# Optimization experiments

Hardware: AMD Instinct MI355X
Metric: run time of the kernel (lower is better)

## Reference

```python
import jax, jax.numpy as jnp
import numpy as np

B = 512
MIRROR_C1_OFFSET = -1.2432432432432432

def make_ff(batch):
    ff = jnp.zeros((1, 1, 60, 60), jnp.float32)
    ff = ff.at[0, 0, :, 41:51].set(0.5)
    ff = ff.at[0, 0, :, 51:].set(1.0)
    return jnp.broadcast_to(ff, (batch, 1, 60, 60))

def conv_valid(x, w, b):
    y = jax.lax.conv_general_dilated(x, w, (1, 1), 'VALID',
                                     dimension_numbers=('NCHW', 'OIHW', 'NCHW'))
    return y + b[None, :, None, None]

def build_padded(x, h, ff):
    # (B,3,92,92) canvas with custom mirror padding (channel-dependent sign on left)
    b = x.shape[0]
    inner = jnp.concatenate([x, h, ff], axis=1)  # (B,3,60,60)
    h2 = jnp.zeros((b, 3, 92, 92), x.dtype)
    h2 = h2.at[:, :, 16:76, 16:76].set(inner)
    h2 = h2.at[:, :, 16:76, 76:].set(h2[:, :, 16:76, 60:76][..., ::-1])
    h2 = h2.at[:, :, 76:, 16:].set(h2[:, :, 60:76, 16:][:, :, ::-1, :])
    h2 = h2.at[:, :, :16, 16:].set(0.0)
    left = h2[:, :, :, 16:32][..., ::-1]  # mirror across col 16
    h2 = h2.at[:, 0, :, :16].set(left[:, 0])
    h2 = h2.at[:, 2, :, :16].set(left[:, 2])
    h2 = h2.at[:, 1, :, :16].set(MIRROR_C1_OFFSET - left[:, 1])
    return h2

def powerlayer(x, h, ff, w1, b1, w2, b2, w3, b3, w4, b4):
    h2 = build_padded(x, h, ff)
    h2 = jax.nn.relu(conv_valid(h2, w1, b1))  # (B,8,84,84)
    h2 = jax.nn.relu(conv_valid(h2, w2, b2))  # (B,8,76,76)
    h2 = jax.nn.relu(conv_valid(h2, w3, b3))  # (B,8,68,68)
    h2 = conv_valid(h2, w4, b4)               # (B,1,60,60)
    return h2

def setup_inputs() -> dict:
    key = jax.random.key(0)
    ks = jax.random.split(key, 10)
    x = jax.random.normal(ks[0], (B, 1, 60, 60), jnp.float32)
    fc_w = jax.random.normal(ks[1], (3600, 3600), jnp.float32) * (1.0 / 60.0)
    fc_b = jax.random.normal(ks[2], (3600,), jnp.float32) * 0.01
    w1 = jax.random.normal(ks[3], (8, 3, 9, 9), jnp.float32) * (1.0 / np.sqrt(3 * 81))
    bC1 = jnp.zeros((8,), jnp.float32)
    w2 = jax.random.normal(ks[4], (8, 8, 9, 9), jnp.float32) * (1.0 / np.sqrt(8 * 81))
    bC2 = jnp.zeros((8,), jnp.float32)
    w3 = jax.random.normal(ks[5], (8, 8, 9, 9), jnp.float32) * (1.0 / np.sqrt(8 * 81))
    bC3 = jnp.zeros((8,), jnp.float32)
    w4 = jax.random.normal(ks[6], (1, 8, 9, 9), jnp.float32) * (1.0 / np.sqrt(8 * 81))
    bC4 = jnp.zeros((1,), jnp.float32)
    return {"x": x, "fc_w": fc_w, "fc_b": fc_b,
            "w1": w1, "bC1": bC1, "w2": w2, "bC2": bC2,
            "w3": w3, "bC3": bC3, "w4": w4, "bC4": bC4}

def reference(x, fc_w, fc_b, w1, bC1, w2, bC2, w3, bC3, w4, bC4):
    b = x.shape[0]
    ff = make_ff(b)
    h = jax.nn.relu(x.reshape(b, 3600) @ fc_w.T + fc_b)
    h = h.reshape(b, 1, 60, 60)
    for _ in range(5):
        h = powerlayer(x, h, ff, w1, bC1, w2, bC2, w3, bC3, w4, bC4)
    return h.reshape(b, 60, 60)
```

## Files before the change

kernel.cpp:

```cpp
#include <hip/hip_runtime.h>

#define B_IMG 512
#define C1OFF (-1.2432432432432432f)

typedef __attribute__((ext_vector_type(2))) float f2;
typedef __attribute__((ext_vector_type(4))) float f4;
typedef __attribute__((ext_vector_type(4), aligned(4))) float f4u;

__device__ __forceinline__ float relu_(float v) { return v > 0.f ? v : 0.f; }
__device__ __forceinline__ f2 mk2(float a, float b) { f2 r; r[0] = a; r[1] = b; return r; }

__device__ __forceinline__ int swz_block(int bid, int nwg) {
    int q = nwg >> 3, r = nwg & 7;
    int xcd = bid & 7, idx = bid >> 3;
    return (xcd < r ? xcd * (q + 1) : r * (q + 1) + (xcd - r) * q) + idx;
}

__device__ __forceinline__ f2 pk_fma_sb0(f2 acc, f2 a, f2 b) {
    asm("v_pk_fma_f32 %0, %1, %2, %0 op_sel:[0,0,0] op_sel_hi:[0,1,1]"
        : "+v"(acc) : "s"(a), "v"(b));
    return acc;
}
__device__ __forceinline__ f2 pk_fma_sb1(f2 acc, f2 a, f2 b) {
    asm("v_pk_fma_f32 %0, %1, %2, %0 op_sel:[1,0,0] op_sel_hi:[1,1,1]"
        : "+v"(acc) : "s"(a), "v"(b));
    return acc;
}
__device__ __forceinline__ f2 pk_fma_vb0(f2 acc, f2 a, f2 b) {
    asm("v_pk_fma_f32 %0, %1, %2, %0 op_sel:[0,0,0] op_sel_hi:[0,1,1]"
        : "+v"(acc) : "v"(a), "v"(b));
    return acc;
}
__device__ __forceinline__ f2 pk_fma_vb1(f2 acc, f2 a, f2 b) {
    asm("v_pk_fma_f32 %0, %1, %2, %0 op_sel:[1,0,0] op_sel_hi:[1,1,1]"
        : "+v"(acc) : "v"(a), "v"(b));
    return acc;
}

#define KSPLIT 5
#define KCH 720

__global__ __launch_bounds__(256) void fc_split(
    const float* __restrict__ X, const float* __restrict__ W,
    float* __restrict__ P)
{
    __shared__ __align__(16) float As[16][68];
    __shared__ __align__(16) float Bs[16][68];
    const int tid = threadIdx.x;
    const int m0 = blockIdx.y * 64;
    const int n0 = blockIdx.x * 64;
    const int ks = blockIdx.z;
    const int kbeg = ks * KCH;
    const int tm = tid >> 4, tn = tid & 15;
    const int lr = tid >> 2;
    const int lk = (tid & 3) << 2;
    const bool bvalid = (n0 + lr) < 3600;
    const float* Arow = X + (size_t)(m0 + lr) * 3600 + lk;
    const float* Brow = W + (size_t)(bvalid ? (n0 + lr) : 0) * 3600 + lk;
    f2 acc2[4][2] = {};
    for (int k0 = kbeg; k0 < kbeg + KCH; k0 += 16) {
        float4 av = *(const float4*)(Arow + k0);
        float4 bv = make_float4(0.f, 0.f, 0.f, 0.f);
        if (bvalid) bv = *(const float4*)(Brow + k0);
        __syncthreads();
        As[lk + 0][lr] = av.x; As[lk + 1][lr] = av.y;
        As[lk + 2][lr] = av.z; As[lk + 3][lr] = av.w;
        Bs[lk + 0][lr] = bv.x; Bs[lk + 1][lr] = bv.y;
        Bs[lk + 2][lr] = bv.z; Bs[lk + 3][lr] = bv.w;
        __syncthreads();
        #pragma unroll
        for (int kk = 0; kk < 16; ++kk) {
            f2 a01 = *(const f2*)&As[kk][tm << 2];
            f2 a23 = *(const f2*)&As[kk][(tm << 2) + 2];
            f2 b01 = *(const f2*)&Bs[kk][tn << 2];
            f2 b23 = *(const f2*)&Bs[kk][(tn << 2) + 2];
            acc2[0][0] = pk_fma_vb0(acc2[0][0], a01, b01);
            acc2[0][1] = pk_fma_vb0(acc2[0][1], a01, b23);
            acc2[1][0] = pk_fma_vb1(acc2[1][0], a01, b01);
            acc2[1][1] = pk_fma_vb1(acc2[1][1], a01, b23);
            acc2[2][0] = pk_fma_vb0(acc2[2][0], a23, b01);
            acc2[2][1] = pk_fma_vb0(acc2[2][1], a23, b23);
            acc2[3][0] = pk_fma_vb1(acc2[3][0], a23, b01);
            acc2[3][1] = pk_fma_vb1(acc2[3][1], a23, b23);
        }
    }
    float* Pk = P + (size_t)ks * 512 * 3600;
    #pragma unroll
    for (int i = 0; i < 4; ++i) {
        int m = m0 + (tm << 2) + i;
        float vals[4] = { acc2[i][0][0], acc2[i][0][1],
                          acc2[i][1][0], acc2[i][1][1] };
        #pragma unroll
        for (int j = 0; j < 4; ++j) {
            int n = n0 + (tn << 2) + j;
            if (n < 3600)
                Pk[(size_t)m * 3600 + n] = vals[j];
        }
    }
}

__global__ __launch_bounds__(256) void fc_reduce(
    const float* __restrict__ P, const float* __restrict__ Bv,
    float* __restrict__ H)
{
    const size_t TOT = (size_t)512 * 3600;
    size_t i4 = (size_t)blockIdx.x * 256 + threadIdx.x;
    if (i4 >= TOT / 4) return;
    size_t off = i4 * 4;
    f4 s = *(const f4*)(P + off);
    #pragma unroll
    for (int ks = 1; ks < KSPLIT; ++ks) {
        f4 v = *(const f4*)(P + (size_t)ks * TOT + off);
        s[0] += v[0]; s[1] += v[1]; s[2] += v[2]; s[3] += v[3];
    }
    int n = (int)(off % 3600);
    f4u bv = *(const f4u*)(Bv + n);
    s[0] = relu_(s[0] + bv[0]); s[1] = relu_(s[1] + bv[1]);
    s[2] = relu_(s[2] + bv[2]); s[3] = relu_(s[3] + bv[3]);
    *(f4*)(H + off) = s;
}

__global__ __launch_bounds__(256) void prep_pk(
    const float* __restrict__ w, int OC, int IC, f2* __restrict__ out)
{
    int n = IC * 9 * OC * 5;
    for (int t = threadIdx.x + blockIdx.x * 256; t < n; t += gridDim.x * 256) {
        int m = t % 5; int rest = t / 5;
        int oc = rest % OC; rest /= OC;
        int ky = rest % 9; int ic = rest / 9;
        const float* ws = w + (((size_t)oc * IC + ic) * 9 + ky) * 9;
        float lo = ws[2 * m];
        float hi = (2 * m + 1 < 9) ? ws[2 * m + 1] : 0.f;
        out[t] = mk2(lo, hi);
    }
}

__device__ __forceinline__ float pad_core(const float* __restrict__ xb,
                                          const float* __restrict__ hb,
                                          int ch, int r, int c)
{
    if (r < 16) return 0.f;
    int rr = (r <= 75) ? r : (151 - r);
    int cc = (c <= 75) ? c : (151 - c);
    int i = rr - 16, j = cc - 16;
    if (ch == 0) return xb[i * 60 + j];
    if (ch == 1) return hb[i * 60 + j];
    return (j >= 51) ? 1.0f : ((j >= 41) ? 0.5f : 0.0f);
}

__device__ __forceinline__ float pad_val(const float* __restrict__ xb,
                                         const float* __restrict__ hb,
                                         int ch, int r, int c)
{
    if (c >= 16) return pad_core(xb, hb, ch, r, c);
    float v = pad_core(xb, hb, ch, r, 31 - c);
    return (ch == 1) ? (C1OFF - v) : v;
}

#define PADN 25392
#define CH1OFF 8464

__global__ __launch_bounds__(256) void pad02_kernel(
    const float* __restrict__ x, float* __restrict__ pad)
{
    const int b = blockIdx.x;
    const float* xb = x + (size_t)b * 3600;
    float* pb = pad + (size_t)b * PADN;
    for (int i = threadIdx.x; i < 2 * 8464; i += 256) {
        int cs = i / 8464;
        int rem = i - cs * 8464;
        int r = rem / 92;
        int c = rem - r * 92;
        int ch = cs * 2;
        pb[(size_t)ch * CH1OFF + rem] = pad_val(xb, nullptr, ch, r, c);
    }
}

__global__ __launch_bounds__(256) void padh_kernel(
    const float* __restrict__ h, float* __restrict__ pad)
{
    const int b = blockIdx.x;
    const float* hb = h + (size_t)b * 3600;
    float* pb = pad + (size_t)b * PADN + CH1OFF;
    for (int i = threadIdx.x; i < 8464; i += 256) {
        int r = i / 92;
        int c = i - r * 92;
        pb[i] = pad_val(nullptr, hb, 1, r, c);
    }
}

#define MKPAIRS(row_)                                                         \
    f4 e0 = *(const f4*)(row_);                                               \
    f4 e1 = *(const f4*)((row_) + 4);                                         \
    f4 e2 = *(const f4*)((row_) + 8);                                         \
    f2 re[6], sh[5];                                                          \
    re[0] = mk2(e0[0], e0[1]); re[1] = mk2(e0[2], e0[3]);                     \
    re[2] = mk2(e1[0], e1[1]); re[3] = mk2(e1[2], e1[3]);                     \
    re[4] = mk2(e2[0], e2[1]); re[5] = mk2(e2[2], e2[3]);                     \
    sh[0] = mk2(e0[1], e0[2]); sh[1] = mk2(e0[3], e1[0]);                     \
    sh[2] = mk2(e1[1], e1[2]); sh[3] = mk2(e1[3], e2[0]);                     \
    sh[4] = mk2(e2[1], e2[2]);

template<int IC, int OC, int IH, bool RELU, bool INIT>
__global__ __launch_bounds__(256, 3) void convP(
    const float* __restrict__ in, const f2* __restrict__ wpk,
    const float* __restrict__ bias, const float* __restrict__ basep,
    float* __restrict__ out, int total, int istride, int chstride, int wstride)
{
    constexpr int IW = IH, OH = IH - 8, OW = OH;
    constexpr int NGX = OW / 4, NPB = OH * NGX;
    const int sb = swz_block(blockIdx.x, gridDim.x);
    const int p0 = sb * 256 + threadIdx.x;
    const bool act = (p0 < total);
    const int p = act ? p0 : (total - 1);
    const int b = p / NPB;
    const int rem = p - b * NPB;
    const int oy = rem / NGX;
    const int x0 = (rem - oy * NGX) * 4;
    const float* ib = in + (size_t)b * istride + (size_t)oy * IW + x0;

    f2 acc[OC][2];
    if (INIT) {
        #pragma unroll
        for (int oc = 0; oc < OC; ++oc) {
            const float* bp = basep + ((size_t)b * OC + oc) * (OH * OW)
                              + (size_t)oy * OW + x0;
            f4 v = *(const f4*)bp;
            acc[oc][0] = mk2(v[0], v[1]);
            acc[oc][1] = mk2(v[2], v[3]);
        }
    } else {
        #pragma unroll
        for (int oc = 0; oc < OC; ++oc) {
            float bv = bias[oc];
            acc[oc][0] = mk2(bv, bv);
            acc[oc][1] = mk2(bv, bv);
        }
    }

    #pragma unroll 1
    for (int ic = 0; ic < IC; ++ic) {
        const float* rp = ib + (size_t)ic * chstride;
        const f2* wq0 = wpk + (size_t)ic * wstride;
        #pragma unroll
        for (int ky = 0; ky < 9; ++ky) {
            const float* row = rp + ky * IW;
            MKPAIRS(row)
            const f2* wq = wq0 + ky * OC * 5;
            #pragma unroll
            for (int oc = 0; oc < OC; ++oc) {
                const f2* w5 = wq + oc * 5;
                #pragma unroll
                for (int m = 0; m < 4; ++m) {
                    f2 w = w5[m];
                    acc[oc][0] = pk_fma_sb0(acc[oc][0], w, re[m]);
                    acc[oc][0] = pk_fma_sb1(acc[oc][0], w, sh[m]);
                    acc[oc][1] = pk_fma_sb0(acc[oc][1], w, re[m + 1]);
                    acc[oc][1] = pk_fma_sb1(acc[oc][1], w, sh[m + 1]);
                }
                f2 w4v = w5[4];
                acc[oc][0] = pk_fma_sb0(acc[oc][0], w4v, re[4]);
                acc[oc][1] = pk_fma_sb0(acc[oc][1], w4v, re[5]);
            }
        }
    }

    if (act) {
        #pragma unroll
        for (int oc = 0; oc < OC; ++oc) {
            float* ob = out + ((size_t)b * OC + oc) * (OH * OW)
                        + (size_t)oy * OW + x0;
            float v0 = acc[oc][0][0], v1 = acc[oc][0][1];
            float v2 = acc[oc][1][0], v3 = acc[oc][1][1];
            if (RELU) { v0 = relu_(v0); v1 = relu_(v1); v2 = relu_(v2); v3 = relu_(v3); }
            *(float4*)ob = make_float4(v0, v1, v2, v3);
        }
    }
}

#define LOADROW(RE, SH, KY)                                                   \
    do {                                                                      \
        const float* row_ = rp + (KY) * IW;                                   \
        f4 e0_ = *(const f4*)(row_);                                          \
        f4 e1_ = *(const f4*)(row_ + 4);                                      \
        f4 e2_ = *(const f4*)(row_ + 8);                                      \
        RE[0] = mk2(e0_[0], e0_[1]); RE[1] = mk2(e0_[2], e0_[3]);             \
        RE[2] = mk2(e1_[0], e1_[1]); RE[3] = mk2(e1_[2], e1_[3]);             \
        RE[4] = mk2(e2_[0], e2_[1]); RE[5] = mk2(e2_[2], e2_[3]);             \
        SH[0] = mk2(e0_[1], e0_[2]); SH[1] = mk2(e0_[3], e1_[0]);             \
        SH[2] = mk2(e1_[1], e1_[2]); SH[3] = mk2(e1_[3], e2_[0]);             \
        SH[4] = mk2(e2_[1], e2_[2]);                                          \
    } while (0)

#define FMASTEP(TRE, TSH, BRE, BSH, KY)                                       \
    do {                                                                      \
        const f2* wq_ = wq0 + (KY) * OC * 5;                                  \
        _Pragma("unroll")                                                     \
        for (int oc = 0; oc < OC; ++oc) {                                     \
            const f2* w5_ = wq_ + oc * 5;                                     \
            _Pragma("unroll")                                                 \
            for (int m = 0; m < 4; ++m) {                                     \
                f2 w_ = w5_[m];                                               \
                acc[oc][0][0] = pk_fma_sb0(acc[oc][0][0], w_, TRE[m]);        \
                acc[oc][0][0] = pk_fma_sb1(acc[oc][0][0], w_, TSH[m]);        \
                acc[oc][0][1] = pk_fma_sb0(acc[oc][0][1], w_, TRE[m + 1]);    \
                acc[oc][0][1] = pk_fma_sb1(acc[oc][0][1], w_, TSH[m + 1]);    \
                acc[oc][1][0] = pk_fma_sb0(acc[oc][1][0], w_, BRE[m]);        \
                acc[oc][1][0] = pk_fma_sb1(acc[oc][1][0], w_, BSH[m]);        \
                acc[oc][1][1] = pk_fma_sb0(acc[oc][1][1], w_, BRE[m + 1]);    \
                acc[oc][1][1] = pk_fma_sb1(acc[oc][1][1], w_, BSH[m + 1]);    \
            }                                                                 \
            f2 w4_ = w5_[4];                                                  \
            acc[oc][0][0] = pk_fma_sb0(acc[oc][0][0], w4_, TRE[4]);           \
            acc[oc][0][1] = pk_fma_sb0(acc[oc][0][1], w4_, TRE[5]);           \
            acc[oc][1][0] = pk_fma_sb0(acc[oc][1][0], w4_, BRE[4]);           \
            acc[oc][1][1] = pk_fma_sb0(acc[oc][1][1], w4_, BRE[5]);           \
        }                                                                     \
    } while (0)

#define STEP(TRE, TSH, BRE, BSH, KY)                                          \
    do { LOADROW(BRE, BSH, (KY) + 1); FMASTEP(TRE, TSH, BRE, BSH, KY); } while (0)

template<int IC, int OC, int IH, bool RELU, bool INIT>
__global__ __launch_bounds__(256, 2) void convP2(
    const float* __restrict__ in, const f2* __restrict__ wpk,
    const float* __restrict__ bias, const float* __restrict__ basep,
    float* __restrict__ out, int total, int istride, int chstride, int wstride)
{
    constexpr int IW = IH, OH = IH - 8, OW = OH;
    constexpr int NGX = OW / 4, NGY = OH / 2, NPB = NGX * NGY;
    const int sb = swz_block(blockIdx.x, gridDim.x);
    const int p0 = sb * 256 + threadIdx.x;
    const bool act = (p0 < total);
    const int p = act ? p0 : (total - 1);
    const int b = p / NPB;
    const int rem = p - b * NPB;
    const int gy = rem / NGX;
    const int gx = rem - gy * NGX;
    const int oy = gy * 2, x0 = gx * 4;
    const float* ib = in + (size_t)b * istride + (size_t)oy * IW + x0;

    f2 acc[OC][2][2];
    if (INIT) {
        #pragma unroll
        for (int oc = 0; oc < OC; ++oc) {
            const float* bp = basep + ((size_t)b * OC + oc) * (OH * OW)
                              + (size_t)oy * OW + x0;
            f4 v0 = *(const f4*)bp;
            f4 v1 = *(const f4*)(bp + OW);
            acc[oc][0][0] = mk2(v0[0], v0[1]); acc[oc][0][1] = mk2(v0[2], v0[3]);
            acc[oc][1][0] = mk2(v1[0], v1[1]); acc[oc][1][1] = mk2(v1[2], v1[3]);
        }
    } else {
        #pragma unroll
        for (int oc = 0; oc < OC; ++oc) {
            float bv = bias[oc];
            acc[oc][0][0] = mk2(bv, bv); acc[oc][0][1] = mk2(bv, bv);
            acc[oc][1][0] = mk2(bv, bv); acc[oc][1][1] = mk2(bv, bv);
        }
    }

    #pragma unroll 1
    for (int ic = 0; ic < IC; ++ic) {
        const float* rp = ib + (size_t)ic * chstride;
        const f2* wq0 = wpk + (size_t)ic * wstride;
        f2 reA[6], shA[5], reB[6], shB[5];
        LOADROW(reA, shA, 0);
        STEP(reA, shA, reB, shB, 0);
        STEP(reB, shB, reA, shA, 1);
        STEP(reA, shA, reB, shB, 2);
        STEP(reB, shB, reA, shA, 3);
        STEP(reA, shA, reB, shB, 4);
        STEP(reB, shB, reA, shA, 5);
        STEP(reA, shA, reB, shB, 6);
        STEP(reB, shB, reA, shA, 7);
        STEP(reA, shA, reB, shB, 8);
    }

    if (act) {
        #pragma unroll
        for (int oc = 0; oc < OC; ++oc) {
            float* ob = out + ((size_t)b * OC + oc) * (OH * OW)
                        + (size_t)oy * OW + x0;
            float v0 = acc[oc][0][0][0], v1 = acc[oc][0][0][1];
            float v2 = acc[oc][0][1][0], v3 = acc[oc][0][1][1];
            float u0 = acc[oc][1][0][0], u1 = acc[oc][1][0][1];
            float u2 = acc[oc][1][1][0], u3 = acc[oc][1][1][1];
            if (RELU) {
                v0 = relu_(v0); v1 = relu_(v1); v2 = relu_(v2); v3 = relu_(v3);
                u0 = relu_(u0); u1 = relu_(u1); u2 = relu_(u2); u3 = relu_(u3);
            }
            *(float4*)&ob[0]  = make_float4(v0, v1, v2, v3);
            *(float4*)&ob[OW] = make_float4(u0, u1, u2, u3);
        }
    }
}

extern "C" void kernel_launch(void* const* d_in, const int* in_sizes, int n_in,
                              void* d_out, int out_size, void* d_ws, size_t ws_size,
                              hipStream_t stream)
{
    const float* x   = (const float*)d_in[0];
    const float* fcw = (const float*)d_in[1];
    const float* fcb = (const float*)d_in[2];
    const float* w1  = (const float*)d_in[3];
    const float* b1  = (const float*)d_in[4];
    const float* w2  = (const float*)d_in[5];
    const float* b2  = (const float*)d_in[6];
    const float* w3  = (const float*)d_in[7];
    const float* b3  = (const float*)d_in[8];
    const float* w4  = (const float*)d_in[9];
    const float* b4  = (const float*)d_in[10];

    float* h = (float*)d_out;

    f2* wp1 = (f2*)d_ws;
    f2* wp2 = wp1 + 4096;
    f2* wp3 = wp2 + 4096;
    f2* wp4 = wp3 + 4096;
    float* region = (float*)((char*)d_ws + 131072);
    size_t avail = (ws_size - 131072) / sizeof(float);

    float* fcp = region;

    const size_t T1N = 8 * 84 * 84;
    const size_t T2N = 8 * 76 * 76;
    size_t per_img = PADN + T1N + T1N + T2N;
    int CHN = (int)(avail / per_img);
    if (CHN > B_IMG) CHN = B_IMG;
    if (CHN < 1) CHN = 1;
    float* pad  = region;
    float* bse  = pad + (size_t)CHN * PADN;
    float* t1   = bse + (size_t)CHN * T1N;
    float* t2   = t1 + (size_t)CHN * T1N;

    prep_pk<<<5, 256, 0, stream>>>(w1, 8, 3, wp1);
    prep_pk<<<12, 256, 0, stream>>>(w2, 8, 8, wp2);
    prep_pk<<<12, 256, 0, stream>>>(w3, 8, 8, wp3);
    prep_pk<<<2, 256, 0, stream>>>(w4, 1, 8, wp4);

    fc_split<<<dim3(57, 8, KSPLIT), 256, 0, stream>>>(x, fcw, fcp);
    fc_reduce<<<1800, 256, 0, stream>>>(fcp, fcb, h);

    for (int c0 = 0; c0 < B_IMG; c0 += CHN) {
        int cn = (B_IMG - c0) < CHN ? (B_IMG - c0) : CHN;
        pad02_kernel<<<cn, 256, 0, stream>>>(x + (size_t)c0 * 3600, pad);
        int tb = cn * 882;
        convP2<2, 8, 92, false, false><<<(tb + 255) / 256, 256, 0, stream>>>(
            pad, wp1, b1, nullptr, bse, tb, PADN, 2 * CH1OFF, 2 * 360);
        for (int it = 0; it < 5; ++it) {
            padh_kernel<<<cn, 256, 0, stream>>>(h + (size_t)c0 * 3600, pad);
            int t1n = cn * 882;
            int t2n = cn * 1444;
            int t3n = cn * 1156;
            int t4n = cn * 450;
            convP2<1, 8, 92, true, true><<<(t1n + 255) / 256, 256, 0, stream>>>(
                pad + CH1OFF, wp1 + 360, nullptr, bse, t1, t1n, PADN, 0, 0);
            convP<8, 8, 84, true, false><<<(t2n + 255) / 256, 256, 0, stream>>>(
                t1, wp2, b2, nullptr, t2, t2n, (int)T1N, 84 * 84, 360);
            convP<8, 8, 76, true, false><<<(t3n + 255) / 256, 256, 0, stream>>>(
                t2, wp3, b3, nullptr, t1, t3n, (int)T2N, 76 * 76, 360);
            convP2<8, 1, 68, false, false><<<(t4n + 255) / 256, 256, 0, stream>>>(
                t1, wp4, b4, nullptr, h + (size_t)c0 * 3600, t4n,
                8 * 68 * 68, 68 * 68, 45);
        }
    }
}
```

Measured before the change: 3.689 ms.

## Fuse padding of h into final conv epilogue and hoist padh out of loop

The last conv of each power layer now writes its output both to h and directly into the padded channel-1 canvas, including the mirrored right, bottom and left regions. The constant top rows are written once in pad02_kernel, and padh_kernel runs only once before the iteration loop. This removes a separate padding launch and its global re-read of h per iteration. The cost is scattered extra stores in the conv4 epilogue, which depend on correct handling of the mirror coordinates.

```diff
diff --git a/kernel.cpp b/kernel.cpp
--- a/kernel.cpp
+++ b/kernel.cpp
@@ -166,13 +166,22 @@
     const int b = blockIdx.x;
     const float* xb = x + (size_t)b * 3600;
     float* pb = pad + (size_t)b * PADN;
-    for (int i = threadIdx.x; i < 2 * 8464; i += 256) {
-        int cs = i / 8464;
-        int rem = i - cs * 8464;
-        int r = rem / 92;
-        int c = rem - r * 92;
-        int ch = cs * 2;
-        pb[(size_t)ch * CH1OFF + rem] = pad_val(xb, nullptr, ch, r, c);
+    const int N02 = 2 * 8464;
+    const int NTOP = 16 * 92;
+    for (int i = threadIdx.x; i < N02 + NTOP; i += 256) {
+        if (i < N02) {
+            int cs = i / 8464;
+            int rem = i - cs * 8464;
+            int r = rem / 92;
+            int c = rem - r * 92;
+            int ch = cs * 2;
+            pb[(size_t)ch * CH1OFF + rem] = pad_val(xb, nullptr, ch, r, c);
+        } else {
+            int j = i - N02;
+            int r = j / 92;
+            int c = j - r * 92;
+            pb[CH1OFF + r * 92 + c] = (c < 16) ? C1OFF : 0.f;
+        }
     }
 }
 
@@ -185,7 +194,7 @@
     for (int i = threadIdx.x; i < 8464; i += 256) {
         int r = i / 92;
         int c = i - r * 92;
-        pb[i] = pad_val(nullptr, hb, 1, r, c);
+        if (r >= 16) pb[i] = pad_val(nullptr, hb, 1, r, c);
     }
 }
 
@@ -396,6 +405,80 @@
     }
 }
 
+__global__ __launch_bounds__(256, 2) void convP4(
+    const float* __restrict__ in, const f2* __restrict__ wpk,
+    const float* __restrict__ bias, float* __restrict__ hout,
+    float* __restrict__ pad, int total)
+{
+    constexpr int OC = 1;
+    constexpr int IH = 68, IW = 68, OW = 60;
+    constexpr int NGX = 15, NPB = 450;
+    const int sb = swz_block(blockIdx.x, gridDim.x);
+    const int p0 = sb * 256 + threadIdx.x;
+    const bool act = (p0 < total);
+    const int p = act ? p0 : (total - 1);
+    const int b = p / NPB;
+    const int rem = p - b * NPB;
+    const int gy = rem / NGX;
+    const int gx = rem - gy * NGX;
+    const int oy = gy * 2, x0 = gx * 4;
+    const float* ib = in + (size_t)b * (8 * 68 * 68) + (size_t)oy * IW + x0;
+
+    f2 acc[OC][2][2];
+    float bv = bias[0];
+    acc[0][0][0] = mk2(bv, bv); acc[0][0][1] = mk2(bv, bv);
+    acc[0][1][0] = mk2(bv, bv); acc[0][1][1] = mk2(bv, bv);
+
+    #pragma unroll 1
+    for (int ic = 0; ic < 8; ++ic) {
+        const float* rp = ib + (size_t)ic * (68 * 68);
+        const f2* wq0 = wpk + (size_t)ic * 45;
+        f2 reA[6], shA[5], reB[6], shB[5];
+        LOADROW(reA, shA, 0);
+        STEP(reA, shA, reB, shB, 0);
+        STEP(reB, shB, reA, shA, 1);
+        STEP(reA, shA, reB, shB, 2);
+        STEP(reB, shB, reA, shA, 3);
+        STEP(reA, shA, reB, shB, 4);
+        STEP(reB, shB, reA, shA, 5);
+        STEP(reA, shA, reB, shB, 6);
+        STEP(reB, shB, reA, shA, 7);
+        STEP(reA, shA, reB, shB, 8);
+    }
+
+    if (act) {
+        float vals[2][4] = {
+            { acc[0][0][0][0], acc[0][0][0][1], acc[0][0][1][0], acc[0][0][1][1] },
+            { acc[0][1][0][0], acc[0][1][0][1], acc[0][1][1][0], acc[0][1][1][1] } };
+        float* hb = hout + (size_t)b * 3600 + (size_t)oy * OW + x0;
+        *(float4*)&hb[0]  = make_float4(vals[0][0], vals[0][1], vals[0][2], vals[0][3]);
+        *(float4*)&hb[OW] = make_float4(vals[1][0], vals[1][1], vals[1][2], vals[1][3]);
+        float* pb = pad + (size_t)b * PADN + CH1OFF;
+        #pragma unroll
+        for (int r2 = 0; r2 < 2; ++r2) {
+            int hr = oy + r2;
+            *(float4*)&pb[(16 + hr) * 92 + 16 + x0] =
+                make_float4(vals[r2][0], vals[r2][1], vals[r2][2], vals[r2][3]);
+            #pragma unroll
+            for (int j = 0; j < 4; ++j) {
+                int hc = x0 + j; float v = vals[r2][j];
+                if (hc <= 15) pb[(16 + hr) * 92 + 15 - hc] = C1OFF - v;
+                if (hc >= 44) pb[(16 + hr) * 92 + 135 - hc] = v;
+            }
+            if (hr >= 44) {
+                int qr = 135 - hr;
+                #pragma unroll
+                for (int j = 0; j < 4; ++j) {
+                    int hc = x0 + j; float v = vals[r2][j];
+                    pb[qr * 92 + 16 + hc] = v;
+                    if (hc <= 15) pb[qr * 92 + 15 - hc] = C1OFF - v;
+                    if (hc >= 44) pb[qr * 92 + 135 - hc] = v;
+                }
+            }
+        }
+    }
+}
+
 extern "C" void kernel_launch(void* const* d_in, const int* in_sizes, int n_in,
                               void* d_out, int out_size, void* d_ws, size_t ws_size,
                               hipStream_t stream)
@@ -448,8 +531,8 @@
         int tb = cn * 882;
         convP2<2, 8, 92, false, false><<<(tb + 255) / 256, 256, 0, stream>>>(
             pad, wp1, b1, nullptr, bse, tb, PADN, 2 * CH1OFF, 2 * 360);
+        padh_kernel<<<cn, 256, 0, stream>>>(h + (size_t)c0 * 3600, pad);
         for (int it = 0; it < 5; ++it) {
-            padh_kernel<<<cn, 256, 0, stream>>>(h + (size_t)c0 * 3600, pad);
             int t1n = cn * 882;
             int t2n = cn * 1444;
             int t3n = cn * 1156;
@@ -460,9 +543,8 @@
                 t1, wp2, b2, nullptr, t2, t2n, (int)T1N, 84 * 84, 360);
             convP<8, 8, 76, true, false><<<(t3n + 255) / 256, 256, 0, stream>>>(
                 t2, wp3, b3, nullptr, t1, t3n, (int)T2N, 76 * 76, 360);
-            convP2<8, 1, 68, false, false><<<(t4n + 255) / 256, 256, 0, stream>>>(
-                t1, wp4, b4, nullptr, h + (size_t)c0 * 3600, t4n,
-                8 * 68 * 68, 68 * 68, 45);
-        }
-    }
-}
+            convP4<<<(t4n + 255) / 256, 256, 0, stream>>>(
+                t1, wp4, b4, h + (size_t)c0 * 3600, pad, t4n);
+        }
+    }
+}
```

After: 3.536 ms. 1.04x faster.
